# Kernel tuning notes

Hardware: AMD Instinct MI355X
Metric: run time of the kernel (lower is better)

Reference implementation:

```python
import jax, jax.numpy as jnp
import numpy as np

N, IN_F, OUT_F = 4096, 4096, 4096
THRESH = 0.05


def setup_inputs() -> dict:
    key = jax.random.key(0)
    k_x, k_w = jax.random.split(key)
    last_out = jax.random.normal(k_x, (N, IN_F), dtype=jnp.float32)
    # learned weight buffer, [out_features, in_features] like torch Linear
    weight = jax.random.normal(k_w, (OUT_F, IN_F), dtype=jnp.float32) * (1.0 / np.sqrt(IN_F))
    threshold = jnp.float32(THRESH)
    return {"last_out": last_out, "weight": weight, "threshold": threshold}


def reference(last_out, weight, threshold):
    # rtp_linear: runtime threshold pruning — activations with |x| <= threshold
    # are skipped (treated as zero) in the matmul. Bias buffer is unused
    # (dead code in the original forward).
    x = jnp.where(jnp.abs(last_out) > threshold, last_out, 0.0)
    # y[n, o] = sum_i x[n, i] * W[o, i]
    return jnp.einsum("ni,oi->no", x, weight)
```

## Files before the change

### kernel.cpp

```cpp
#include <hip/hip_runtime.h>
#include <hip/hip_bf16.h>

#define M_DIM 4096
#define N_DIM 4096
#define K_DIM 4096

typedef __attribute__((ext_vector_type(8))) __bf16 bf16x8;
typedef __attribute__((ext_vector_type(8))) short short8;
typedef __attribute__((ext_vector_type(8))) unsigned short ushort8;
typedef __attribute__((ext_vector_type(4))) float f32x4;

__device__ __forceinline__ void gload_lds16(const void* g, void* l) {
    __builtin_amdgcn_global_load_lds(
        (const __attribute__((address_space(1))) void*)g,
        (__attribute__((address_space(3))) void*)l,
        16, 0, 0);
}

__device__ __forceinline__ bf16x8 ld8(const unsigned short* p) {
    short8 r = *reinterpret_cast<const short8*>(p);
    return __builtin_bit_cast(bf16x8, r);
}

__global__ void prune_cvt2(const float* __restrict__ x,
                           const float* __restrict__ w,
                           unsigned short* __restrict__ xb,
                           unsigned short* __restrict__ wb,
                           const float* __restrict__ thrp, int n8) {
    const float thr = thrp[0];
    const int stride = gridDim.x * blockDim.x;
    const int total = 2 * n8;
    for (int idx = blockIdx.x * blockDim.x + threadIdx.x; idx < total; idx += stride) {
        const bool isx = idx < n8;
        const int j = isx ? idx : idx - n8;
        const float* src = isx ? x : w;
        unsigned short* dst = isx ? xb : wb;
        const float te = isx ? thr : -1.0f;
        const float4* p = reinterpret_cast<const float4*>(src) + 2 * (size_t)j;
        float4 v0 = p[0];
        float4 v1 = p[1];
        float v[8] = {v0.x, v0.y, v0.z, v0.w, v1.x, v1.y, v1.z, v1.w};
        ushort8 o;
#pragma unroll
        for (int e = 0; e < 8; ++e) {
            float f = v[e];
            f = (fabsf(f) > te) ? f : 0.0f;
            __hip_bfloat16 hh = __float2bfloat16(f);
            o[e] = *reinterpret_cast<unsigned short*>(&hh);
        }
        *reinterpret_cast<ushort8*>(dst + 8 * (size_t)j) = o;
    }
}

__global__ __launch_bounds__(512, 2) void gemm_8phase(
        const unsigned short* __restrict__ A,
        const unsigned short* __restrict__ B,
        float* __restrict__ C) {
    __shared__ __align__(16) unsigned short lds[65536];

    const int tid  = threadIdx.x;
    const int lane = tid & 63;
    const int wid  = tid >> 6;
    const int wr   = wid >> 2;
    const int wc   = wid & 3;

    const int bid = blockIdx.x;
    const int swz = (bid & 7) * 32 + (bid >> 3);
    const int bm = (swz >> 4) * 256;
    const int bn = (swz & 15) * 256;

    const int g  = tid & 255;
    const int ah = tid >> 8;
    const int arow = bm + ah * 128 + (g >> 3);
    const int acol = 8 * ((g & 7) ^ ((g >> 3) & 7));
    const unsigned short* Asrc = A + (size_t)arow * K_DIM + acol;
    const int AdstE = ah * 8192 + g * 8;

    const int h = lane + 64 * wr;
    const int brow = bn + wc * 64 + (h >> 3);
    const int bcol = 8 * ((h & 7) ^ ((h >> 3) & 7));
    const unsigned short* Bsrc = B + (size_t)brow * K_DIM + bcol;
    const int BdstE = wc * 4096 + h * 8;

#define SA(dstb, j, kg) gload_lds16(Asrc + (size_t)(32*(j))*K_DIM + (kg), (dstb) + AdstE + 2048*(j))
#define SB(dstb, j, kg) gload_lds16(Bsrc + (size_t)(16*(j))*K_DIM + (kg), (dstb) + BdstE + 1024*(j))

    const int fr  = lane & 15;
    const int kq4 = lane >> 4;
    const int rowOffA = (wr * 128 + fr) * 64;
    const int rowOffB = (wc * 64 + fr) * 64;
    const int sk0 = 8 * ((kq4    ) ^ (fr & 7));
    const int sk1 = 8 * ((kq4 + 4) ^ (fr & 7));

    f32x4 acc[8][4] = {};

    bf16x8 bfr[4][2];
#define MFMA16(q, A00, A10, A01, A11)                                                              \
    __builtin_amdgcn_s_setprio(1);                                                                 \
    _Pragma("unroll")                                                                              \
    for (int n = 0; n < 4; ++n) {                                                                  \
        acc[2*(q)][n]   = __builtin_amdgcn_mfma_f32_16x16x32_bf16(A00, bfr[n][0], acc[2*(q)][n], 0, 0, 0);   \
        acc[2*(q)+1][n] = __builtin_amdgcn_mfma_f32_16x16x32_bf16(A10, bfr[n][0], acc[2*(q)+1][n], 0, 0, 0); \
    }                                                                                              \
    _Pragma("unroll")                                                                              \
    for (int n = 0; n < 4; ++n) {                                                                  \
        acc[2*(q)][n]   = __builtin_amdgcn_mfma_f32_16x16x32_bf16(A01, bfr[n][1], acc[2*(q)][n], 0, 0, 0);   \
        acc[2*(q)+1][n] = __builtin_amdgcn_mfma_f32_16x16x32_bf16(A11, bfr[n][1], acc[2*(q)+1][n], 0, 0, 0); \
    }                                                                                              \
    __builtin_amdgcn_s_setprio(0);

#define TILE_BODY(Ab, Bb, AbN, BbN, kn)                                                            \
    {                                                                                              \
                                        \
        _Pragma("unroll")                                                                          \
        for (int n = 0; n < 4; ++n) {                                                              \
            bfr[n][0] = ld8((Bb) + rowOffB + n * 1024 + sk0);                                      \
            bfr[n][1] = ld8((Bb) + rowOffB + n * 1024 + sk1);                                      \
        }                                                                                          \
        bf16x8 q00 = ld8((Ab) + rowOffA + 2 * 1024 + sk0);                                         \
        bf16x8 q10 = ld8((Ab) + rowOffA + 3 * 1024 + sk0);                                         \
        bf16x8 q01 = ld8((Ab) + rowOffA + 2 * 1024 + sk1);                                         \
        bf16x8 q11 = ld8((Ab) + rowOffA + 3 * 1024 + sk1);                                         \
        SB((BbN), 0, (kn)); SB((BbN), 1, (kn)); SB((BbN), 2, (kn)); SB((BbN), 3, (kn));            \
        MFMA16(0, p00, p10, p01, p11);                                                             \
        asm volatile("s_waitcnt vmcnt(5)" ::: "memory");                                           \
        asm volatile("s_barrier" ::: "memory");                                                    \
                                            \
        bf16x8 r00 = ld8((Ab) + rowOffA + 4 * 1024 + sk0);                                         \
        bf16x8 r10 = ld8((Ab) + rowOffA + 5 * 1024 + sk0);                                         \
        bf16x8 r01 = ld8((Ab) + rowOffA + 4 * 1024 + sk1);                                         \
        bf16x8 r11 = ld8((Ab) + rowOffA + 5 * 1024 + sk1);                                         \
        SA((AbN), 0, (kn)); SA((AbN), 1, (kn));                                                    \
        MFMA16(1, q00, q10, q01, q11);                                                             \
        asm volatile("s_waitcnt vmcnt(6)" ::: "memory");                                           \
        asm volatile("s_barrier" ::: "memory");                                                    \
                                            \
        bf16x8 s00 = ld8((Ab) + rowOffA + 6 * 1024 + sk0);                                         \
        bf16x8 s10 = ld8((Ab) + rowOffA + 7 * 1024 + sk0);                                         \
        bf16x8 s01 = ld8((Ab) + rowOffA + 6 * 1024 + sk1);                                         \
        bf16x8 s11 = ld8((Ab) + rowOffA + 7 * 1024 + sk1);                                         \
        SA((AbN), 2, (kn)); SA((AbN), 3, (kn));                                                    \
        MFMA16(2, r00, r10, r01, r11);                                                             \
        asm volatile("s_waitcnt vmcnt(3)" ::: "memory");                                           \
        asm volatile("s_barrier" ::: "memory");                                                    \
                                       \
        p00 = ld8((AbN) + rowOffA + 0 * 1024 + sk0);                                               \
        p10 = ld8((AbN) + rowOffA + 1 * 1024 + sk0);                                               \
        p01 = ld8((AbN) + rowOffA + 0 * 1024 + sk1);                                               \
        p11 = ld8((AbN) + rowOffA + 1 * 1024 + sk1);                                               \
        MFMA16(3, s00, s10, s01, s11);                                                             \
        asm volatile("s_waitcnt vmcnt(2)" ::: "memory");                                           \
        asm volatile("s_barrier" ::: "memory");                                                    \
    }

    unsigned short* A0 = lds;
    unsigned short* A1 = lds + 16384;
    unsigned short* B0 = lds + 32768;
    unsigned short* B1 = lds + 49152;

    SB(B0, 0, 0); SB(B0, 1, 0); SB(B0, 2, 0); SB(B0, 3, 0);
    SA(A0, 0, 0); SA(A0, 1, 0); SA(A0, 2, 0); SA(A0, 3, 0);
    asm volatile("s_waitcnt vmcnt(2)" ::: "memory");
    asm volatile("s_barrier" ::: "memory");

    bf16x8 p00 = ld8(A0 + rowOffA + 0 * 1024 + sk0);
    bf16x8 p10 = ld8(A0 + rowOffA + 1 * 1024 + sk0);
    bf16x8 p01 = ld8(A0 + rowOffA + 0 * 1024 + sk1);
    bf16x8 p11 = ld8(A0 + rowOffA + 1 * 1024 + sk1);

    for (int t = 0; t < 64; t += 2) {
        const int kn0 = (t + 1) * 64;
        const int kn1 = (t + 2 < 64 ? t + 2 : 63) * 64;
        TILE_BODY(A0, B0, A1, B1, kn0);
        TILE_BODY(A1, B1, A0, B0, kn1);
    }

    asm volatile("s_waitcnt vmcnt(0)" ::: "memory");

    const int crow = bm + wr * 128 + kq4 * 4;
    const int ccol = bn + wc * 64 + fr;
#pragma unroll
    for (int m = 0; m < 8; ++m)
#pragma unroll
        for (int n = 0; n < 4; ++n)
#pragma unroll
            for (int j = 0; j < 4; ++j)
                C[(size_t)(crow + m * 16 + j) * N_DIM + ccol + n * 16] = acc[m][n][j];
}

__global__ void gemm_f32_fallback(const float* __restrict__ A,
                                  const float* __restrict__ B,
                                  float* __restrict__ C,
                                  const float* __restrict__ thrp) {
    __shared__ float As[32][33];
    __shared__ float Bs[32][33];
    const float thr = thrp[0];
    const int tx = threadIdx.x, ty = threadIdx.y;
    const int row = blockIdx.y * 32 + ty;
    float acc = 0.0f;
    for (int k0 = 0; k0 < K_DIM; k0 += 32) {
        float a = A[(size_t)row * K_DIM + k0 + tx];
        As[ty][tx] = (fabsf(a) > thr) ? a : 0.0f;
        Bs[ty][tx] = B[(size_t)(blockIdx.x * 32 + ty) * K_DIM + k0 + tx];
        __syncthreads();
#pragma unroll 8
        for (int kk = 0; kk < 32; ++kk)
            acc += As[ty][kk] * Bs[tx][kk];
        __syncthreads();
    }
    C[(size_t)row * N_DIM + blockIdx.x * 32 + tx] = acc;
}

extern "C" void kernel_launch(void* const* d_in, const int* in_sizes, int n_in,
                              void* d_out, int out_size, void* d_ws, size_t ws_size,
                              hipStream_t stream) {
    const float* x    = (const float*)d_in[0];
    const float* w    = (const float*)d_in[1];
    const float* thrp = (const float*)d_in[2];
    float* out = (float*)d_out;

    const size_t elems = (size_t)M_DIM * K_DIM;
    if (ws_size >= 2 * elems * sizeof(unsigned short)) {
        unsigned short* Ab = (unsigned short*)d_ws;
        unsigned short* Bb = Ab + elems;
        const int n8 = (int)(elems / 8);
        prune_cvt2<<<2048, 256, 0, stream>>>(x, w, Ab, Bb, thrp, n8);
        gemm_8phase<<<dim3(256), dim3(512), 0, stream>>>(Ab, Bb, out);
    } else {
        dim3 grid(N_DIM / 32, M_DIM / 32), blk(32, 32);
        gemm_f32_fallback<<<grid, blk, 0, stream>>>(x, w, out, thrp);
    }
}
```

Before: 144.7 us.

## Fuse threshold pruning and bf16 conversion into GEMM tile loading

```diff
diff --git a/kernel.cpp b/kernel.cpp
--- a/kernel.cpp
+++ b/kernel.cpp
@@ -10,54 +10,32 @@
 typedef __attribute__((ext_vector_type(8))) unsigned short ushort8;
 typedef __attribute__((ext_vector_type(4))) float f32x4;
 
-__device__ __forceinline__ void gload_lds16(const void* g, void* l) {
-    __builtin_amdgcn_global_load_lds(
-        (const __attribute__((address_space(1))) void*)g,
-        (__attribute__((address_space(3))) void*)l,
-        16, 0, 0);
-}
-
 __device__ __forceinline__ bf16x8 ld8(const unsigned short* p) {
     short8 r = *reinterpret_cast<const short8*>(p);
     return __builtin_bit_cast(bf16x8, r);
 }
 
-__global__ void prune_cvt2(const float* __restrict__ x,
-                           const float* __restrict__ w,
-                           unsigned short* __restrict__ xb,
-                           unsigned short* __restrict__ wb,
-                           const float* __restrict__ thrp, int n8) {
-    const float thr = thrp[0];
-    const int stride = gridDim.x * blockDim.x;
-    const int total = 2 * n8;
-    for (int idx = blockIdx.x * blockDim.x + threadIdx.x; idx < total; idx += stride) {
-        const bool isx = idx < n8;
-        const int j = isx ? idx : idx - n8;
-        const float* src = isx ? x : w;
-        unsigned short* dst = isx ? xb : wb;
-        const float te = isx ? thr : -1.0f;
-        const float4* p = reinterpret_cast<const float4*>(src) + 2 * (size_t)j;
-        float4 v0 = p[0];
-        float4 v1 = p[1];
-        float v[8] = {v0.x, v0.y, v0.z, v0.w, v1.x, v1.y, v1.z, v1.w};
-        ushort8 o;
+__device__ __forceinline__ ushort8 cvt8(float4 a, float4 b, float thr) {
+    float v[8] = {a.x, a.y, a.z, a.w, b.x, b.y, b.z, b.w};
+    ushort8 o;
 #pragma unroll
-        for (int e = 0; e < 8; ++e) {
-            float f = v[e];
-            f = (fabsf(f) > te) ? f : 0.0f;
-            __hip_bfloat16 hh = __float2bfloat16(f);
-            o[e] = *reinterpret_cast<unsigned short*>(&hh);
-        }
-        *reinterpret_cast<ushort8*>(dst + 8 * (size_t)j) = o;
+    for (int e = 0; e < 8; ++e) {
+        float f = v[e];
+        f = (fabsf(f) > thr) ? f : 0.0f;
+        __hip_bfloat16 h = __float2bfloat16(f);
+        o[e] = *reinterpret_cast<unsigned short*>(&h);
     }
+    return o;
 }
 
-__global__ __launch_bounds__(512, 2) void gemm_8phase(
-        const unsigned short* __restrict__ A,
-        const unsigned short* __restrict__ B,
+__global__ __launch_bounds__(512, 2) void gemm_fused(
+        const float* __restrict__ X,
+        const float* __restrict__ W,
+        const float* __restrict__ thrp,
         float* __restrict__ C) {
     __shared__ __align__(16) unsigned short lds[65536];
 
+    const float thr = thrp[0];
     const int tid  = threadIdx.x;
     const int lane = tid & 63;
     const int wid  = tid >> 6;
@@ -69,21 +47,16 @@
     const int bm = (swz >> 4) * 256;
     const int bn = (swz & 15) * 256;
 
-    const int g  = tid & 255;
-    const int ah = tid >> 8;
-    const int arow = bm + ah * 128 + (g >> 3);
-    const int acol = 8 * ((g & 7) ^ ((g >> 3) & 7));
-    const unsigned short* Asrc = A + (size_t)arow * K_DIM + acol;
-    const int AdstE = ah * 8192 + g * 8;
+    const int sx = tid & 7;
+    const int rb = tid >> 3;
+    const float* xbase = X + (size_t)(bm + rb) * K_DIM + sx * 8;
+    const float* wbase = W + (size_t)(bn + rb) * K_DIM + sx * 8;
+    const int dstoff = rb * 64 + 8 * (sx ^ (rb & 7));
 
-    const int h = lane + 64 * wr;
-    const int brow = bn + wc * 64 + (h >> 3);
-    const int bcol = 8 * ((h & 7) ^ ((h >> 3) & 7));
-    const unsigned short* Bsrc = B + (size_t)brow * K_DIM + bcol;
-    const int BdstE = wc * 4096 + h * 8;
-
-#define SA(dstb, j, kg) gload_lds16(Asrc + (size_t)(32*(j))*K_DIM + (kg), (dstb) + AdstE + 2048*(j))
-#define SB(dstb, j, kg) gload_lds16(Bsrc + (size_t)(16*(j))*K_DIM + (kg), (dstb) + BdstE + 1024*(j))
+#define LDF4(base, kn, k, half) \
+    (*reinterpret_cast<const float4*>((base) + (kn) + (size_t)(k) * 64 * K_DIM + 4 * (half)))
+#define STW(dstb, k, u) \
+    (*reinterpret_cast<ushort8*>((dstb) + dstoff + 4096 * (k)) = (u))
 
     const int fr  = lane & 15;
     const int kq4 = lane >> 4;
@@ -93,8 +66,8 @@
     const int sk1 = 8 * ((kq4 + 4) ^ (fr & 7));
 
     f32x4 acc[8][4] = {};
+    bf16x8 bfr[4][2];
 
-    bf16x8 bfr[4][2];
 #define MFMA16(q, A00, A10, A01, A11)                                                              \
     __builtin_amdgcn_s_setprio(1);                                                                 \
     _Pragma("unroll")                                                                              \
@@ -111,45 +84,52 @@
 
 #define TILE_BODY(Ab, Bb, AbN, BbN, kn)                                                            \
     {                                                                                              \
-                                        \
+                                  \
         _Pragma("unroll")                                                                          \
         for (int n = 0; n < 4; ++n) {                                                              \
             bfr[n][0] = ld8((Bb) + rowOffB + n * 1024 + sk0);                                      \
             bfr[n][1] = ld8((Bb) + rowOffB + n * 1024 + sk1);                                      \
         }                                                                                          \
+        bf16x8 p00 = ld8((Ab) + rowOffA + 0 * 1024 + sk0);                                         \
+        bf16x8 p10 = ld8((Ab) + rowOffA + 1 * 1024 + sk0);                                         \
+        bf16x8 p01 = ld8((Ab) + rowOffA + 0 * 1024 + sk1);                                         \
+        bf16x8 p11 = ld8((Ab) + rowOffA + 1 * 1024 + sk1);                                         \
         bf16x8 q00 = ld8((Ab) + rowOffA + 2 * 1024 + sk0);                                         \
         bf16x8 q10 = ld8((Ab) + rowOffA + 3 * 1024 + sk0);                                         \
         bf16x8 q01 = ld8((Ab) + rowOffA + 2 * 1024 + sk1);                                         \
         bf16x8 q11 = ld8((Ab) + rowOffA + 3 * 1024 + sk1);                                         \
-        SB((BbN), 0, (kn)); SB((BbN), 1, (kn)); SB((BbN), 2, (kn)); SB((BbN), 3, (kn));            \
+        float4 a0l = LDF4(xbase, kn, 0, 0), a0h = LDF4(xbase, kn, 0, 1);                           \
+        float4 a1l = LDF4(xbase, kn, 1, 0), a1h = LDF4(xbase, kn, 1, 1);                           \
         MFMA16(0, p00, p10, p01, p11);                                                             \
-        asm volatile("s_waitcnt vmcnt(5)" ::: "memory");                                           \
-        asm volatile("s_barrier" ::: "memory");                                                    \
-                                            \
+                                        \
         bf16x8 r00 = ld8((Ab) + rowOffA + 4 * 1024 + sk0);                                         \
         bf16x8 r10 = ld8((Ab) + rowOffA + 5 * 1024 + sk0);                                         \
         bf16x8 r01 = ld8((Ab) + rowOffA + 4 * 1024 + sk1);                                         \
         bf16x8 r11 = ld8((Ab) + rowOffA + 5 * 1024 + sk1);                                         \
-        SA((AbN), 0, (kn)); SA((AbN), 1, (kn));                                                    \
+        STW((AbN), 0, cvt8(a0l, a0h, thr));                                                        \
+        STW((AbN), 1, cvt8(a1l, a1h, thr));                                                        \
+        float4 a2l = LDF4(xbase, kn, 2, 0), a2h = LDF4(xbase, kn, 2, 1);                           \
+        float4 a3l = LDF4(xbase, kn, 3, 0), a3h = LDF4(xbase, kn, 3, 1);                           \
         MFMA16(1, q00, q10, q01, q11);                                                             \
-        asm volatile("s_waitcnt vmcnt(6)" ::: "memory");                                           \
-        asm volatile("s_barrier" ::: "memory");                                                    \
-                                            \
+                                       \
         bf16x8 s00 = ld8((Ab) + rowOffA + 6 * 1024 + sk0);                                         \
         bf16x8 s10 = ld8((Ab) + rowOffA + 7 * 1024 + sk0);                                         \
         bf16x8 s01 = ld8((Ab) + rowOffA + 6 * 1024 + sk1);                                         \
         bf16x8 s11 = ld8((Ab) + rowOffA + 7 * 1024 + sk1);                                         \
-        SA((AbN), 2, (kn)); SA((AbN), 3, (kn));                                                    \
+        STW((AbN), 2, cvt8(a2l, a2h, thr));                                                        \
+        STW((AbN), 3, cvt8(a3l, a3h, thr));                                                        \
+        float4 b0l = LDF4(wbase, kn, 0, 0), b0h = LDF4(wbase, kn, 0, 1);                           \
+        float4 b1l = LDF4(wbase, kn, 1, 0), b1h = LDF4(wbase, kn, 1, 1);                           \
+        float4 b2l = LDF4(wbase, kn, 2, 0), b2h = LDF4(wbase, kn, 2, 1);                           \
+        float4 b3l = LDF4(wbase, kn, 3, 0), b3h = LDF4(wbase, kn, 3, 1);                           \
         MFMA16(2, r00, r10, r01, r11);                                                             \
-        asm volatile("s_waitcnt vmcnt(3)" ::: "memory");                                           \
-        asm volatile("s_barrier" ::: "memory");                                                    \
-                                       \
-        p00 = ld8((AbN) + rowOffA + 0 * 1024 + sk0);                                               \
-        p10 = ld8((AbN) + rowOffA + 1 * 1024 + sk0);                                               \
-        p01 = ld8((AbN) + rowOffA + 0 * 1024 + sk1);                                               \
-        p11 = ld8((AbN) + rowOffA + 1 * 1024 + sk1);                                               \
+                                                \
+        STW((BbN), 0, cvt8(b0l, b0h, -1.0f));                                                      \
+        STW((BbN), 1, cvt8(b1l, b1h, -1.0f));                                                      \
+        STW((BbN), 2, cvt8(b2l, b2h, -1.0f));                                                      \
+        STW((BbN), 3, cvt8(b3l, b3h, -1.0f));                                                      \
         MFMA16(3, s00, s10, s01, s11);                                                             \
-        asm volatile("s_waitcnt vmcnt(2)" ::: "memory");                                           \
+        asm volatile("s_waitcnt lgkmcnt(0)" ::: "memory");                                         \
         asm volatile("s_barrier" ::: "memory");                                                    \
     }
 
@@ -158,15 +138,26 @@
     unsigned short* B0 = lds + 32768;
     unsigned short* B1 = lds + 49152;
 
-    SB(B0, 0, 0); SB(B0, 1, 0); SB(B0, 2, 0); SB(B0, 3, 0);
-    SA(A0, 0, 0); SA(A0, 1, 0); SA(A0, 2, 0); SA(A0, 3, 0);
-    asm volatile("s_waitcnt vmcnt(2)" ::: "memory");
-    asm volatile("s_barrier" ::: "memory");
-
-    bf16x8 p00 = ld8(A0 + rowOffA + 0 * 1024 + sk0);
-    bf16x8 p10 = ld8(A0 + rowOffA + 1 * 1024 + sk0);
-    bf16x8 p01 = ld8(A0 + rowOffA + 0 * 1024 + sk1);
-    bf16x8 p11 = ld8(A0 + rowOffA + 1 * 1024 + sk1);
+    {
+        float4 a0l = LDF4(xbase, 0, 0, 0), a0h = LDF4(xbase, 0, 0, 1);
+        float4 a1l = LDF4(xbase, 0, 1, 0), a1h = LDF4(xbase, 0, 1, 1);
+        float4 a2l = LDF4(xbase, 0, 2, 0), a2h = LDF4(xbase, 0, 2, 1);
+        float4 a3l = LDF4(xbase, 0, 3, 0), a3h = LDF4(xbase, 0, 3, 1);
+        float4 b0l = LDF4(wbase, 0, 0, 0), b0h = LDF4(wbase, 0, 0, 1);
+        float4 b1l = LDF4(wbase, 0, 1, 0), b1h = LDF4(wbase, 0, 1, 1);
+        float4 b2l = LDF4(wbase, 0, 2, 0), b2h = LDF4(wbase, 0, 2, 1);
+        float4 b3l = LDF4(wbase, 0, 3, 0), b3h = LDF4(wbase, 0, 3, 1);
+        STW(A0, 0, cvt8(a0l, a0h, thr));
+        STW(A0, 1, cvt8(a1l, a1h, thr));
+        STW(A0, 2, cvt8(a2l, a2h, thr));
+        STW(A0, 3, cvt8(a3l, a3h, thr));
+        STW(B0, 0, cvt8(b0l, b0h, -1.0f));
+        STW(B0, 1, cvt8(b1l, b1h, -1.0f));
+        STW(B0, 2, cvt8(b2l, b2h, -1.0f));
+        STW(B0, 3, cvt8(b3l, b3h, -1.0f));
+        asm volatile("s_waitcnt lgkmcnt(0)" ::: "memory");
+        asm volatile("s_barrier" ::: "memory");
+    }
 
     for (int t = 0; t < 64; t += 2) {
         const int kn0 = (t + 1) * 64;
@@ -174,8 +165,6 @@
         TILE_BODY(A0, B0, A1, B1, kn0);
         TILE_BODY(A1, B1, A0, B0, kn1);
     }
-
-    asm volatile("s_waitcnt vmcnt(0)" ::: "memory");
 
     const int crow = bm + wr * 128 + kq4 * 4;
     const int ccol = bn + wc * 64 + fr;
@@ -188,29 +177,6 @@
                 C[(size_t)(crow + m * 16 + j) * N_DIM + ccol + n * 16] = acc[m][n][j];
 }
 
-__global__ void gemm_f32_fallback(const float* __restrict__ A,
-                                  const float* __restrict__ B,
-                                  float* __restrict__ C,
-                                  const float* __restrict__ thrp) {
-    __shared__ float As[32][33];
-    __shared__ float Bs[32][33];
-    const float thr = thrp[0];
-    const int tx = threadIdx.x, ty = threadIdx.y;
-    const int row = blockIdx.y * 32 + ty;
-    float acc = 0.0f;
-    for (int k0 = 0; k0 < K_DIM; k0 += 32) {
-        float a = A[(size_t)row * K_DIM + k0 + tx];
-        As[ty][tx] = (fabsf(a) > thr) ? a : 0.0f;
-        Bs[ty][tx] = B[(size_t)(blockIdx.x * 32 + ty) * K_DIM + k0 + tx];
-        __syncthreads();
-#pragma unroll 8
-        for (int kk = 0; kk < 32; ++kk)
-            acc += As[ty][kk] * Bs[tx][kk];
-        __syncthreads();
-    }
-    C[(size_t)row * N_DIM + blockIdx.x * 32 + tx] = acc;
-}
-
 extern "C" void kernel_launch(void* const* d_in, const int* in_sizes, int n_in,
                               void* d_out, int out_size, void* d_ws, size_t ws_size,
                               hipStream_t stream) {
@@ -218,16 +184,7 @@
     const float* w    = (const float*)d_in[1];
     const float* thrp = (const float*)d_in[2];
     float* out = (float*)d_out;
+    (void)d_ws; (void)ws_size;
 
-    const size_t elems = (size_t)M_DIM * K_DIM;
-    if (ws_size >= 2 * elems * sizeof(unsigned short)) {
-        unsigned short* Ab = (unsigned short*)d_ws;
-        unsigned short* Bb = Ab + elems;
-        const int n8 = (int)(elems / 8);
-        prune_cvt2<<<2048, 256, 0, stream>>>(x, w, Ab, Bb, thrp, n8);
-        gemm_8phase<<<dim3(256), dim3(512), 0, stream>>>(Ab, Bb, out);
-    } else {
-        dim3 grid(N_DIM / 32, M_DIM / 32), blk(32, 32);
-        gemm_f32_fallback<<<grid, blk, 0, stream>>>(x, w, out, thrp);
-    }
+    gemm_fused<<<dim3(256), dim3(512), 0, stream>>>(x, w, thrp, out);
 }
```

New measurement: 177.5 us. 1.23x slower.
